# Kernel optimization log

Measured on AMD Instinct MI355X. Metric: run time of the kernel, lower is better.

The kernel has to match this reference:

```python
import jax, jax.numpy as jnp
import numpy as np

N_NODES = 50000
N_EDGES = 800000
IN_C, HID_C, OUT_C = 128, 96, 64
BN_EPS = 1e-5


def setup_inputs() -> dict:
    key = jax.random.key(0)
    ks = jax.random.split(key, 12)
    x = jax.random.normal(ks[0], (N_NODES, IN_C), dtype=jnp.float32)
    edge_weight = jax.random.uniform(ks[1], (N_EDGES,), dtype=jnp.float32)
    row = jax.random.randint(ks[2], (N_EDGES,), 0, N_NODES, dtype=jnp.int32)
    col = jax.random.randint(ks[3], (N_EDGES,), 0, N_NODES, dtype=jnp.int32)
    s = 0.05
    W1 = jax.random.normal(ks[4], (IN_C, HID_C), dtype=jnp.float32) * s
    b1 = jnp.zeros((HID_C,), dtype=jnp.float32)
    W2 = jax.random.normal(ks[5], (HID_C, HID_C), dtype=jnp.float32) * s
    b2 = jnp.zeros((HID_C,), dtype=jnp.float32)
    W3 = jax.random.normal(ks[6], (HID_C, OUT_C), dtype=jnp.float32) * s
    b3 = jnp.zeros((OUT_C,), dtype=jnp.float32)
    g1 = jnp.ones((HID_C,), dtype=jnp.float32)
    be1 = jnp.zeros((HID_C,), dtype=jnp.float32)
    g2 = jnp.ones((HID_C,), dtype=jnp.float32)
    be2 = jnp.zeros((HID_C,), dtype=jnp.float32)
    return {"x": x, "edge_weight": edge_weight, "row": row, "col": col,
            "W1": W1, "b1": b1, "W2": W2, "b2": b2, "W3": W3, "b3": b3,
            "g1": g1, "be1": be1, "g2": g2, "be2": be2}


def _gcn_conv(h, edge_weight, row, col, W, b):
    # GCNConv: adj_norm @ (h @ W) + b, adj in COO with normalized edge_weight
    h = h @ W  # [N, d_out]
    msg = edge_weight[:, None] * h[col]  # gather + scale: [E, d_out]
    agg = jax.ops.segment_sum(msg, row, num_segments=N_NODES)  # scatter-add
    return agg + b


def _batch_norm(h, gamma, beta):
    # BatchNorm1d (training-mode batch statistics, biased variance)
    mean = jnp.mean(h, axis=0)
    var = jnp.var(h, axis=0)
    return (h - mean) * jax.lax.rsqrt(var + BN_EPS) * gamma + beta


def reference(x, edge_weight, row, col, W1, b1, W2, b2, W3, b3, g1, be1, g2, be2):
    h = _gcn_conv(x, edge_weight, row, col, W1, b1)
    h = jax.nn.relu(_batch_norm(h, g1, be1))  # dropout is identity in eval
    h = _gcn_conv(h, edge_weight, row, col, W2, b2)
    h = jax.nn.relu(_batch_norm(h, g2, be2))
    h = _gcn_conv(h, edge_weight, row, col, W3, b3)
    return jax.nn.log_softmax(h, axis=-1)
```

## Files before the change

kernel.cpp:

```cpp
#include <hip/hip_runtime.h>
#include <hip/hip_bf16.h>
#include <math.h>

#define N_NODES 50000
#define N_EDGES 800000
#define IN_C 128
#define HID_C 96
#define OUT_C 64
#define BN_EPS 1e-5f

#define ELL_SHIFT 6
#define ELL_CAP   64

#define NGRP 8
#define GRP_ROWS ((N_NODES + NGRP - 1) / NGRP)

#define EW_SCALE 65535.0f
#define EW_INV   (1.0f / 65535.0f)

#define ST_SLICES 4

typedef __attribute__((ext_vector_type(8))) short short8;
typedef __attribute__((ext_vector_type(4))) float f32x4;

static __device__ __forceinline__ unsigned short f2b(float f) {
    __hip_bfloat16 b = __float2bfloat16(f);
    return *reinterpret_cast<unsigned short*>(&b);
}
static __device__ __forceinline__ float b2f(unsigned short u) {
    return __uint_as_float((unsigned)u << 16);
}
static __device__ __forceinline__ unsigned pack2(float a, float b) {
    return (unsigned)f2b(a) | ((unsigned)f2b(b) << 16);
}

#define FMA8(B, V, W)                                          \
    acc[(B) + 0] += (W) * __uint_as_float((V).x << 16);        \
    acc[(B) + 1] += (W) * __uint_as_float((V).x & 0xffff0000u);\
    acc[(B) + 2] += (W) * __uint_as_float((V).y << 16);        \
    acc[(B) + 3] += (W) * __uint_as_float((V).y & 0xffff0000u);\
    acc[(B) + 4] += (W) * __uint_as_float((V).z << 16);        \
    acc[(B) + 5] += (W) * __uint_as_float((V).z & 0xffff0000u);\
    acc[(B) + 6] += (W) * __uint_as_float((V).w << 16);        \
    acc[(B) + 7] += (W) * __uint_as_float((V).w & 0xffff0000u);

__global__ void prep_all(const float* __restrict__ W1, const float* __restrict__ W2,
                         const float* __restrict__ W3,
                         unsigned short* __restrict__ Wt1,
                         unsigned short* __restrict__ Wt2,
                         unsigned short* __restrict__ Wt3,
                         int* __restrict__ cnt, float* __restrict__ stats) {
    int i = blockIdx.x * blockDim.x + threadIdx.x;
    const int n1 = IN_C * HID_C, n2 = HID_C * HID_C, n3 = HID_C * OUT_C;
    if (i < n1) {
        int j = i / IN_C, k = i % IN_C;
        Wt1[i] = f2b(W1[k * HID_C + j]);
    } else if (i < n1 + n2) {
        int t = i - n1, j = t / HID_C, k = t % HID_C;
        Wt2[t] = f2b(W2[k * HID_C + j]);
    } else if (i < n1 + n2 + n3) {
        int t = i - n1 - n2, j = t / HID_C, k = t % HID_C;
        Wt3[t] = f2b(W3[k * OUT_C + j]);
    }
    if (i < N_NODES) cnt[i] = 0;
    if (i < 2 * ST_SLICES * 2 * HID_C) stats[i] = 0.f;
}

__global__ __launch_bounds__(256)
void fill_ell(const int* __restrict__ row, const int* __restrict__ col,
              const float* __restrict__ ew, int* __restrict__ cnt,
              unsigned int* __restrict__ pairs) {
    int g = blockIdx.x & (NGRP - 1);
    int e = (blockIdx.x >> 3) * 256 + threadIdx.x;
    if (e >= N_EDGES) return;
    int r = row[e];
    int lo = g * GRP_ROWS;
    if ((unsigned)(r - lo) >= (unsigned)GRP_ROWS) return;
    int slot = atomicAdd(&cnt[r], 1);
    if (slot < ELL_CAP) {
        unsigned wq = (unsigned)(ew[e] * EW_SCALE + 0.5f);
        pairs[((size_t)r << ELL_SHIFT) + slot] =
            (wq << 16) | (unsigned)col[e];
    }
}

template <int K, int J, bool APPLY, bool XBF16>
__global__ __launch_bounds__(256)
void gemm_mfma(const void* __restrict__ xin,
               const unsigned short* __restrict__ Wt,
               const float* __restrict__ stats,
               const float* __restrict__ gamma,
               const float* __restrict__ beta,
               unsigned short* __restrict__ h, int N) {
    constexpr int MT = 64;
    constexpr int SK = K + 8;
    constexpr int NT = J / 16;
    __shared__ unsigned short Xs[MT * SK];
    __shared__ unsigned short Ws[J * SK];
    __shared__ float scsh_s[APPLY ? 2 * K : 2];

    int tid = threadIdx.x;
    int tileBase = blockIdx.x * MT;

    if (APPLY) {
        if (tid < K) {
            float s = 0.f, sq = 0.f;
#pragma unroll
            for (int sl = 0; sl < ST_SLICES; ++sl) {
                s  += stats[sl * 2 * K + tid];
                sq += stats[sl * 2 * K + K + tid];
            }
            const float invN = 1.f / N_NODES;
            float mean = s * invN;
            float var = sq * invN - mean * mean;
            float sc = gamma[tid] * rsqrtf(var + BN_EPS);
            scsh_s[tid] = sc;
            scsh_s[K + tid] = beta[tid] - mean * sc;
        }
        __syncthreads();
    }

    if (XBF16) {
        const unsigned short* xb = (const unsigned short*)xin;
        for (int i = tid; i < MT * (K / 8); i += 256) {
            int node = i / (K / 8), kq = i % (K / 8);
            int gn = min(tileBase + node, N - 1);
            const unsigned short* src = xb + (size_t)gn * K + kq * 8;
            ushort4 u0 = *(const ushort4*)(src);
            ushort4 u1 = *(const ushort4*)(src + 4);
            if (APPLY) {
                int kb = kq * 8;
                float v0 = fmaxf(b2f(u0.x) * scsh_s[kb + 0] + scsh_s[K + kb + 0], 0.f);
                float v1 = fmaxf(b2f(u0.y) * scsh_s[kb + 1] + scsh_s[K + kb + 1], 0.f);
                float v2 = fmaxf(b2f(u0.z) * scsh_s[kb + 2] + scsh_s[K + kb + 2], 0.f);
                float v3 = fmaxf(b2f(u0.w) * scsh_s[kb + 3] + scsh_s[K + kb + 3], 0.f);
                float v4 = fmaxf(b2f(u1.x) * scsh_s[kb + 4] + scsh_s[K + kb + 4], 0.f);
                float v5 = fmaxf(b2f(u1.y) * scsh_s[kb + 5] + scsh_s[K + kb + 5], 0.f);
                float v6 = fmaxf(b2f(u1.z) * scsh_s[kb + 6] + scsh_s[K + kb + 6], 0.f);
                float v7 = fmaxf(b2f(u1.w) * scsh_s[kb + 7] + scsh_s[K + kb + 7], 0.f);
                u0 = make_ushort4(f2b(v0), f2b(v1), f2b(v2), f2b(v3));
                u1 = make_ushort4(f2b(v4), f2b(v5), f2b(v6), f2b(v7));
            }
            *(ushort4*)&Xs[node * SK + kq * 8] = u0;
            *(ushort4*)&Xs[node * SK + kq * 8 + 4] = u1;
        }
    } else {
        const float* xf = (const float*)xin;
        for (int i = tid; i < MT * (K / 4); i += 256) {
            int node = i / (K / 4), kq = i % (K / 4);
            int gn = min(tileBase + node, N - 1);
            float4 v = *(const float4*)(xf + (size_t)gn * K + kq * 4);
            ushort4 o = make_ushort4(f2b(v.x), f2b(v.y), f2b(v.z), f2b(v.w));
            *(ushort4*)&Xs[node * SK + kq * 4] = o;
        }
    }
    for (int i = tid; i < J * (K / 4); i += 256) {
        int j = i / (K / 4), kq = i % (K / 4);
        *(ushort4*)&Ws[j * SK + kq * 4] =
            *(const ushort4*)(Wt + (size_t)j * K + kq * 4);
    }
    __syncthreads();

    int lane = tid & 63;
    int w = tid >> 6;
    int m16 = lane & 15;
    int quad = lane >> 4;

    f32x4 acc[NT];
#pragma unroll
    for (int nt = 0; nt < NT; ++nt) acc[nt] = (f32x4){0.f, 0.f, 0.f, 0.f};

    const unsigned short* xrow = &Xs[(w * 16 + m16) * SK];
#pragma unroll
    for (int k0 = 0; k0 < K; k0 += 32) {
        short8 a = *(const short8*)(xrow + k0 + quad * 8);
#pragma unroll
        for (int nt = 0; nt < NT; ++nt) {
            short8 b = *(const short8*)&Ws[(nt * 16 + m16) * SK + k0 + quad * 8];
            acc[nt] = __builtin_amdgcn_mfma_f32_16x16x32_bf16(a, b, acc[nt], 0, 0, 0);
        }
    }

#pragma unroll
    for (int nt = 0; nt < NT; ++nt) {
#pragma unroll
        for (int r = 0; r < 4; ++r) {
            int node = tileBase + w * 16 + quad * 4 + r;
            if (node < N)
                h[(size_t)node * J + nt * 16 + m16] = f2b(acc[nt][r]);
        }
    }
}

template <int D, bool LSM, bool STATS>
__global__ __launch_bounds__(256)
void agg_fused(const unsigned short* __restrict__ h,
               const int* __restrict__ cnt,
               const unsigned int* __restrict__ pairs,
               unsigned short* __restrict__ outb,
               float* __restrict__ outf,
               const float* __restrict__ b3,
               float* __restrict__ stats) {
    constexpr int TPN = 4;
    constexpr int C = D / TPN;
    constexpr int NPB = 256 / TPN;
    __shared__ float shS[STATS ? 16 * C : 1];
    __shared__ float shQ[STATS ? 16 * C : 1];

    int tid = threadIdx.x;
    int q = tid & 3;
    int nloc = tid >> 2;
    int n = blockIdx.x * NPB + nloc;
    bool valid = n < N_NODES;
    int nn = valid ? n : N_NODES - 1;
    int end = valid ? min(cnt[nn], ELL_CAP) : 0;
    const unsigned* ep = pairs + ((size_t)nn << ELL_SHIFT);
    const int cbase = q * C;

    float acc[C];
#pragma unroll
    for (int c = 0; c < C; ++c) acc[c] = 0.f;

    int i = 0;
    for (; i + 1 < end; i += 2) {
        unsigned p0 = ep[i], p1 = ep[i + 1];
        float w0 = (float)(p0 >> 16) * EW_INV;
        float w1 = (float)(p1 >> 16) * EW_INV;
        const unsigned short* r0 = h + (size_t)(p0 & 0xFFFFu) * D + cbase;
        const unsigned short* r1 = h + (size_t)(p1 & 0xFFFFu) * D + cbase;
        uint4 v0[C / 8], v1[C / 8];
#pragma unroll
        for (int ch = 0; ch < C / 8; ++ch) v0[ch] = *(const uint4*)(r0 + ch * 8);
#pragma unroll
        for (int ch = 0; ch < C / 8; ++ch) v1[ch] = *(const uint4*)(r1 + ch * 8);
#pragma unroll
        for (int ch = 0; ch < C / 8; ++ch) { FMA8(ch * 8, v0[ch], w0) }
#pragma unroll
        for (int ch = 0; ch < C / 8; ++ch) { FMA8(ch * 8, v1[ch], w1) }
    }
    if (i < end) {
        unsigned p0 = ep[i];
        float w0 = (float)(p0 >> 16) * EW_INV;
        const unsigned short* r0 = h + (size_t)(p0 & 0xFFFFu) * D + cbase;
#pragma unroll
        for (int ch = 0; ch < C / 8; ++ch) {
            uint4 v = *(const uint4*)(r0 + ch * 8);
            FMA8(ch * 8, v, w0)
        }
    }

    if (LSM) {
        float v[C];
#pragma unroll
        for (int c = 0; c < C; ++c) v[c] = acc[c] + b3[cbase + c];
        float m = v[0];
#pragma unroll
        for (int c = 1; c < C; ++c) m = fmaxf(m, v[c]);
        m = fmaxf(m, __shfl_xor(m, 1));
        m = fmaxf(m, __shfl_xor(m, 2));
        float s = 0.f;
#pragma unroll
        for (int c = 0; c < C; ++c) s += expf(v[c] - m);
        s += __shfl_xor(s, 1);
        s += __shfl_xor(s, 2);
        float l = m + logf(s);
        if (valid) {
#pragma unroll
            for (int ch = 0; ch < C / 4; ++ch) {
                float4 o = make_float4(v[ch * 4 + 0] - l, v[ch * 4 + 1] - l,
                                       v[ch * 4 + 2] - l, v[ch * 4 + 3] - l);
                *(float4*)(outf + (size_t)n * D + cbase + ch * 4) = o;
            }
        }
    } else {
#pragma unroll
        for (int c = 0; c < C; ++c) acc[c] = b2f(f2b(acc[c]));
#pragma unroll
        for (int ch = 0; ch < C / 8; ++ch) {
            uint4 o;
            o.x = pack2(acc[ch * 8 + 0], acc[ch * 8 + 1]);
            o.y = pack2(acc[ch * 8 + 2], acc[ch * 8 + 3]);
            o.z = pack2(acc[ch * 8 + 4], acc[ch * 8 + 5]);
            o.w = pack2(acc[ch * 8 + 6], acc[ch * 8 + 7]);
            if (valid)
                *(uint4*)(outb + (size_t)n * D + cbase + ch * 8) = o;
        }
        if (STATS) {
            int lane = tid & 63;
            int wv = tid >> 6;
#pragma unroll
            for (int c = 0; c < C; ++c) {
                float s = acc[c];
                float sq = s * s;
#pragma unroll
                for (int msk = 4; msk < 64; msk <<= 1) {
                    s  += __shfl_xor(s, msk);
                    sq += __shfl_xor(sq, msk);
                }
                if (lane < 4) {
                    shS[(wv * 4 + lane) * C + c] = s;
                    shQ[(wv * 4 + lane) * C + c] = sq;
                }
            }
            __syncthreads();
            if (tid < D) {
                int qq = tid / C, cl = tid % C;
                float S = 0.f, Q = 0.f;
#pragma unroll
                for (int w2 = 0; w2 < 4; ++w2) {
                    S += shS[(w2 * 4 + qq) * C + cl];
                    Q += shQ[(w2 * 4 + qq) * C + cl];
                }
                int slice = blockIdx.x & (ST_SLICES - 1);
                atomicAdd(&stats[slice * 2 * D + tid], S);
                atomicAdd(&stats[slice * 2 * D + D + tid], Q);
            }
        }
    }
}

extern "C" void kernel_launch(void* const* d_in, const int* in_sizes, int n_in,
                              void* d_out, int out_size, void* d_ws, size_t ws_size,
                              hipStream_t stream) {
    const float* x   = (const float*)d_in[0];
    const float* ew  = (const float*)d_in[1];
    const int*   row = (const int*)d_in[2];
    const int*   col = (const int*)d_in[3];
    const float* W1  = (const float*)d_in[4];
    const float* W2  = (const float*)d_in[6];
    const float* W3  = (const float*)d_in[8];
    const float* b3  = (const float*)d_in[9];
    const float* g1  = (const float*)d_in[10];
    const float* be1 = (const float*)d_in[11];
    const float* g2  = (const float*)d_in[12];
    const float* be2 = (const float*)d_in[13];
    float* out = (float*)d_out;

    unsigned short* B      = (unsigned short*)d_ws;
    unsigned short* A      = B + (size_t)N_NODES * HID_C;
    unsigned short* Wt1    = A + (size_t)N_NODES * HID_C;
    unsigned short* Wt2    = Wt1 + IN_C * HID_C;
    unsigned short* Wt3    = Wt2 + HID_C * HID_C;
    unsigned int*   pairs  = (unsigned int*)(Wt3 + HID_C * OUT_C);
    int*            cnt    = (int*)(pairs + ((size_t)N_NODES << ELL_SHIFT));
    float*          stats1 = (float*)(cnt + N_NODES);
    float*          stats2 = stats1 + ST_SLICES * 2 * HID_C;

    const int T = 256;
    const int gridE  = (N_EDGES + T - 1) / T;
    const int gridG  = (N_NODES + 63) / 64;
    const int gridP  = (N_NODES + T - 1) / T;

    prep_all<<<gridP, T, 0, stream>>>(W1, W2, W3, Wt1, Wt2, Wt3, cnt, stats1);
    fill_ell<<<gridE * NGRP, T, 0, stream>>>(row, col, ew, cnt, pairs);

    gemm_mfma<IN_C, HID_C, false, false><<<gridG, T, 0, stream>>>(
        x, Wt1, nullptr, nullptr, nullptr, A, N_NODES);
    agg_fused<HID_C, false, true><<<gridG, T, 0, stream>>>(
        A, cnt, pairs, B, nullptr, nullptr, stats1);

    gemm_mfma<HID_C, HID_C, true, true><<<gridG, T, 0, stream>>>(
        B, Wt2, stats1, g1, be1, A, N_NODES);
    agg_fused<HID_C, false, true><<<gridG, T, 0, stream>>>(
        A, cnt, pairs, B, nullptr, nullptr, stats2);

    gemm_mfma<HID_C, OUT_C, true, true><<<gridG, T, 0, stream>>>(
        B, Wt3, stats2, g2, be2, A, N_NODES);
    agg_fused<OUT_C, true, false><<<gridG, T, 0, stream>>>(
        A, cnt, pairs, nullptr, out, b3, nullptr);
}
```

Before: 266.2 us.

## Split aggregation into specialized kernels with eight threads per node and 4-edge unroll

```diff
diff --git a/kernel.cpp b/kernel.cpp
--- a/kernel.cpp
+++ b/kernel.cpp
@@ -43,6 +43,12 @@
     acc[(B) + 5] += (W) * __uint_as_float((V).z & 0xffff0000u);\
     acc[(B) + 6] += (W) * __uint_as_float((V).w << 16);        \
     acc[(B) + 7] += (W) * __uint_as_float((V).w & 0xffff0000u);
+
+#define FMA4(B, V, W)                                          \
+    acc[(B) + 0] += (W) * __uint_as_float((V).x << 16);        \
+    acc[(B) + 1] += (W) * __uint_as_float((V).x & 0xffff0000u);\
+    acc[(B) + 2] += (W) * __uint_as_float((V).y << 16);        \
+    acc[(B) + 3] += (W) * __uint_as_float((V).y & 0xffff0000u);
 
 __global__ void prep_all(const float* __restrict__ W1, const float* __restrict__ W2,
                          const float* __restrict__ W3,
@@ -79,8 +85,7 @@
     int slot = atomicAdd(&cnt[r], 1);
     if (slot < ELL_CAP) {
         unsigned wq = (unsigned)(ew[e] * EW_SCALE + 0.5f);
-        pairs[((size_t)r << ELL_SHIFT) + slot] =
-            (wq << 16) | (unsigned)col[e];
+        pairs[((size_t)r << ELL_SHIFT) + slot] = (wq << 16) | (unsigned)col[e];
     }
 }
 
@@ -192,25 +197,17 @@
     }
 }
 
-template <int D, bool LSM, bool STATS>
 __global__ __launch_bounds__(256)
-void agg_fused(const unsigned short* __restrict__ h,
-               const int* __restrict__ cnt,
-               const unsigned int* __restrict__ pairs,
-               unsigned short* __restrict__ outb,
-               float* __restrict__ outf,
-               const float* __restrict__ b3,
-               float* __restrict__ stats) {
-    constexpr int TPN = 4;
-    constexpr int C = D / TPN;
-    constexpr int NPB = 256 / TPN;
-    __shared__ float shS[STATS ? 16 * C : 1];
-    __shared__ float shQ[STATS ? 16 * C : 1];
-
+void agg96(const unsigned short* __restrict__ h,
+           const int* __restrict__ cnt,
+           const unsigned int* __restrict__ pairs,
+           unsigned short* __restrict__ outb,
+           float* __restrict__ stats) {
+    constexpr int D = HID_C, C = 12;
     int tid = threadIdx.x;
-    int q = tid & 3;
-    int nloc = tid >> 2;
-    int n = blockIdx.x * NPB + nloc;
+    int q = tid & 7;
+    int nloc = tid >> 3;
+    int n = blockIdx.x * 32 + nloc;
     bool valid = n < N_NODES;
     int nn = valid ? n : N_NODES - 1;
     int end = valid ? min(cnt[nn], ELL_CAP) : 0;
@@ -222,100 +219,139 @@
     for (int c = 0; c < C; ++c) acc[c] = 0.f;
 
     int i = 0;
-    for (; i + 1 < end; i += 2) {
-        unsigned p0 = ep[i], p1 = ep[i + 1];
-        float w0 = (float)(p0 >> 16) * EW_INV;
-        float w1 = (float)(p1 >> 16) * EW_INV;
-        const unsigned short* r0 = h + (size_t)(p0 & 0xFFFFu) * D + cbase;
-        const unsigned short* r1 = h + (size_t)(p1 & 0xFFFFu) * D + cbase;
-        uint4 v0[C / 8], v1[C / 8];
-#pragma unroll
-        for (int ch = 0; ch < C / 8; ++ch) v0[ch] = *(const uint4*)(r0 + ch * 8);
-#pragma unroll
-        for (int ch = 0; ch < C / 8; ++ch) v1[ch] = *(const uint4*)(r1 + ch * 8);
-#pragma unroll
-        for (int ch = 0; ch < C / 8; ++ch) { FMA8(ch * 8, v0[ch], w0) }
-#pragma unroll
-        for (int ch = 0; ch < C / 8; ++ch) { FMA8(ch * 8, v1[ch], w1) }
-    }
-    if (i < end) {
-        unsigned p0 = ep[i];
-        float w0 = (float)(p0 >> 16) * EW_INV;
-        const unsigned short* r0 = h + (size_t)(p0 & 0xFFFFu) * D + cbase;
-#pragma unroll
-        for (int ch = 0; ch < C / 8; ++ch) {
-            uint4 v = *(const uint4*)(r0 + ch * 8);
-            FMA8(ch * 8, v, w0)
-        }
-    }
-
-    if (LSM) {
-        float v[C];
-#pragma unroll
-        for (int c = 0; c < C; ++c) v[c] = acc[c] + b3[cbase + c];
-        float m = v[0];
-#pragma unroll
-        for (int c = 1; c < C; ++c) m = fmaxf(m, v[c]);
-        m = fmaxf(m, __shfl_xor(m, 1));
-        m = fmaxf(m, __shfl_xor(m, 2));
-        float s = 0.f;
-#pragma unroll
-        for (int c = 0; c < C; ++c) s += expf(v[c] - m);
-        s += __shfl_xor(s, 1);
-        s += __shfl_xor(s, 2);
-        float l = m + logf(s);
-        if (valid) {
-#pragma unroll
-            for (int ch = 0; ch < C / 4; ++ch) {
-                float4 o = make_float4(v[ch * 4 + 0] - l, v[ch * 4 + 1] - l,
-                                       v[ch * 4 + 2] - l, v[ch * 4 + 3] - l);
-                *(float4*)(outf + (size_t)n * D + cbase + ch * 4) = o;
-            }
-        }
-    } else {
-#pragma unroll
-        for (int c = 0; c < C; ++c) acc[c] = b2f(f2b(acc[c]));
-#pragma unroll
-        for (int ch = 0; ch < C / 8; ++ch) {
-            uint4 o;
-            o.x = pack2(acc[ch * 8 + 0], acc[ch * 8 + 1]);
-            o.y = pack2(acc[ch * 8 + 2], acc[ch * 8 + 3]);
-            o.z = pack2(acc[ch * 8 + 4], acc[ch * 8 + 5]);
-            o.w = pack2(acc[ch * 8 + 6], acc[ch * 8 + 7]);
-            if (valid)
-                *(uint4*)(outb + (size_t)n * D + cbase + ch * 8) = o;
-        }
-        if (STATS) {
-            int lane = tid & 63;
-            int wv = tid >> 6;
-#pragma unroll
-            for (int c = 0; c < C; ++c) {
-                float s = acc[c];
-                float sq = s * s;
-#pragma unroll
-                for (int msk = 4; msk < 64; msk <<= 1) {
-                    s  += __shfl_xor(s, msk);
-                    sq += __shfl_xor(sq, msk);
-                }
-                if (lane < 4) {
-                    shS[(wv * 4 + lane) * C + c] = s;
-                    shQ[(wv * 4 + lane) * C + c] = sq;
-                }
-            }
-            __syncthreads();
-            if (tid < D) {
-                int qq = tid / C, cl = tid % C;
-                float S = 0.f, Q = 0.f;
-#pragma unroll
-                for (int w2 = 0; w2 < 4; ++w2) {
-                    S += shS[(w2 * 4 + qq) * C + cl];
-                    Q += shQ[(w2 * 4 + qq) * C + cl];
-                }
-                int slice = blockIdx.x & (ST_SLICES - 1);
-                atomicAdd(&stats[slice * 2 * D + tid], S);
-                atomicAdd(&stats[slice * 2 * D + D + tid], Q);
-            }
-        }
+    for (; i + 3 < end; i += 4) {
+        uint4 p = *(const uint4*)(ep + i);
+        float w0 = (float)(p.x >> 16) * EW_INV;
+        float w1 = (float)(p.y >> 16) * EW_INV;
+        float w2 = (float)(p.z >> 16) * EW_INV;
+        float w3 = (float)(p.w >> 16) * EW_INV;
+        const unsigned short* r0 = h + (size_t)(p.x & 0xFFFFu) * D + cbase;
+        const unsigned short* r1 = h + (size_t)(p.y & 0xFFFFu) * D + cbase;
+        const unsigned short* r2 = h + (size_t)(p.z & 0xFFFFu) * D + cbase;
+        const unsigned short* r3 = h + (size_t)(p.w & 0xFFFFu) * D + cbase;
+        uint2 a0 = *(const uint2*)(r0), a1 = *(const uint2*)(r0 + 4), a2 = *(const uint2*)(r0 + 8);
+        uint2 b0 = *(const uint2*)(r1), b1 = *(const uint2*)(r1 + 4), b2 = *(const uint2*)(r1 + 8);
+        uint2 c0 = *(const uint2*)(r2), c1 = *(const uint2*)(r2 + 4), c2 = *(const uint2*)(r2 + 8);
+        uint2 d0 = *(const uint2*)(r3), d1 = *(const uint2*)(r3 + 4), d2 = *(const uint2*)(r3 + 8);
+        FMA4(0, a0, w0) FMA4(4, a1, w0) FMA4(8, a2, w0)
+        FMA4(0, b0, w1) FMA4(4, b1, w1) FMA4(8, b2, w1)
+        FMA4(0, c0, w2) FMA4(4, c1, w2) FMA4(8, c2, w2)
+        FMA4(0, d0, w3) FMA4(4, d1, w3) FMA4(8, d2, w3)
+    }
+    for (; i < end; ++i) {
+        unsigned p = ep[i];
+        float w = (float)(p >> 16) * EW_INV;
+        const unsigned short* r0 = h + (size_t)(p & 0xFFFFu) * D + cbase;
+        uint2 a0 = *(const uint2*)(r0), a1 = *(const uint2*)(r0 + 4), a2 = *(const uint2*)(r0 + 8);
+        FMA4(0, a0, w) FMA4(4, a1, w) FMA4(8, a2, w)
+    }
+
+#pragma unroll
+    for (int c = 0; c < C; ++c) acc[c] = b2f(f2b(acc[c]));
+
+    if (valid) {
+        unsigned short* dst = outb + (size_t)n * D + cbase;
+        uint2 o0, o1, o2;
+        o0.x = pack2(acc[0], acc[1]);   o0.y = pack2(acc[2], acc[3]);
+        o1.x = pack2(acc[4], acc[5]);   o1.y = pack2(acc[6], acc[7]);
+        o2.x = pack2(acc[8], acc[9]);   o2.y = pack2(acc[10], acc[11]);
+        *(uint2*)(dst) = o0; *(uint2*)(dst + 4) = o1; *(uint2*)(dst + 8) = o2;
+    }
+
+    __shared__ float shS[4 * 8 * C];
+    __shared__ float shQ[4 * 8 * C];
+    int lane = tid & 63, wv = tid >> 6;
+#pragma unroll
+    for (int c = 0; c < C; ++c) {
+        float s = acc[c];
+        float sq = s * s;
+        s  += __shfl_xor(s, 8);  sq += __shfl_xor(sq, 8);
+        s  += __shfl_xor(s, 16); sq += __shfl_xor(sq, 16);
+        s  += __shfl_xor(s, 32); sq += __shfl_xor(sq, 32);
+        if (lane < 8) { shS[(wv * 8 + lane) * C + c] = s;
+                        shQ[(wv * 8 + lane) * C + c] = sq; }
+    }
+    __syncthreads();
+    if (tid < D) {
+        int qq = tid / C, cl = tid % C;
+        float S = 0.f, Q = 0.f;
+#pragma unroll
+        for (int w2 = 0; w2 < 4; ++w2) {
+            S += shS[(w2 * 8 + qq) * C + cl];
+            Q += shQ[(w2 * 8 + qq) * C + cl];
+        }
+        int sl = blockIdx.x & (ST_SLICES - 1);
+        atomicAdd(&stats[sl * 2 * D + tid], S);
+        atomicAdd(&stats[sl * 2 * D + D + tid], Q);
+    }
+}
+
+__global__ __launch_bounds__(256)
+void agg64_lsm(const unsigned short* __restrict__ h,
+               const int* __restrict__ cnt,
+               const unsigned int* __restrict__ pairs,
+               float* __restrict__ outf,
+               const float* __restrict__ b3) {
+    constexpr int D = OUT_C, C = 8;
+    int tid = threadIdx.x;
+    int q = tid & 7;
+    int nloc = tid >> 3;
+    int n = blockIdx.x * 32 + nloc;
+    bool valid = n < N_NODES;
+    int nn = valid ? n : N_NODES - 1;
+    int end = valid ? min(cnt[nn], ELL_CAP) : 0;
+    const unsigned* ep = pairs + ((size_t)nn << ELL_SHIFT);
+    const int cbase = q * C;
+
+    float acc[C];
+#pragma unroll
+    for (int c = 0; c < C; ++c) acc[c] = 0.f;
+
+    int i = 0;
+    for (; i + 3 < end; i += 4) {
+        uint4 p = *(const uint4*)(ep + i);
+        float w0 = (float)(p.x >> 16) * EW_INV;
+        float w1 = (float)(p.y >> 16) * EW_INV;
+        float w2 = (float)(p.z >> 16) * EW_INV;
+        float w3 = (float)(p.w >> 16) * EW_INV;
+        uint4 v0 = *(const uint4*)(h + (size_t)(p.x & 0xFFFFu) * D + cbase);
+        uint4 v1 = *(const uint4*)(h + (size_t)(p.y & 0xFFFFu) * D + cbase);
+        uint4 v2 = *(const uint4*)(h + (size_t)(p.z & 0xFFFFu) * D + cbase);
+        uint4 v3 = *(const uint4*)(h + (size_t)(p.w & 0xFFFFu) * D + cbase);
+        FMA8(0, v0, w0)
+        FMA8(0, v1, w1)
+        FMA8(0, v2, w2)
+        FMA8(0, v3, w3)
+    }
+    for (; i < end; ++i) {
+        unsigned p = ep[i];
+        float w = (float)(p >> 16) * EW_INV;
+        uint4 v = *(const uint4*)(h + (size_t)(p & 0xFFFFu) * D + cbase);
+        FMA8(0, v, w)
+    }
+
+    float v[C];
+#pragma unroll
+    for (int c = 0; c < C; ++c) v[c] = acc[c] + b3[cbase + c];
+    float m = v[0];
+#pragma unroll
+    for (int c = 1; c < C; ++c) m = fmaxf(m, v[c]);
+    m = fmaxf(m, __shfl_xor(m, 1));
+    m = fmaxf(m, __shfl_xor(m, 2));
+    m = fmaxf(m, __shfl_xor(m, 4));
+    float s = 0.f;
+#pragma unroll
+    for (int c = 0; c < C; ++c) s += expf(v[c] - m);
+    s += __shfl_xor(s, 1);
+    s += __shfl_xor(s, 2);
+    s += __shfl_xor(s, 4);
+    float l = m + logf(s);
+    if (valid) {
+        float4 o0 = make_float4(v[0] - l, v[1] - l, v[2] - l, v[3] - l);
+        float4 o1 = make_float4(v[4] - l, v[5] - l, v[6] - l, v[7] - l);
+        float* dst = outf + (size_t)n * D + cbase;
+        *(float4*)(dst) = o0;
+        *(float4*)(dst + 4) = o1;
     }
 }
 
@@ -349,6 +385,7 @@
     const int T = 256;
     const int gridE  = (N_EDGES + T - 1) / T;
     const int gridG  = (N_NODES + 63) / 64;
+    const int gridA  = (N_NODES + 31) / 32;
     const int gridP  = (N_NODES + T - 1) / T;
 
     prep_all<<<gridP, T, 0, stream>>>(W1, W2, W3, Wt1, Wt2, Wt3, cnt, stats1);
@@ -356,16 +393,13 @@
 
     gemm_mfma<IN_C, HID_C, false, false><<<gridG, T, 0, stream>>>(
         x, Wt1, nullptr, nullptr, nullptr, A, N_NODES);
-    agg_fused<HID_C, false, true><<<gridG, T, 0, stream>>>(
-        A, cnt, pairs, B, nullptr, nullptr, stats1);
+    agg96<<<gridA, T, 0, stream>>>(A, cnt, pairs, B, stats1);
 
     gemm_mfma<HID_C, HID_C, true, true><<<gridG, T, 0, stream>>>(
         B, Wt2, stats1, g1, be1, A, N_NODES);
-    agg_fused<HID_C, false, true><<<gridG, T, 0, stream>>>(
-        A, cnt, pairs, B, nullptr, nullptr, stats2);
+    agg96<<<gridA, T, 0, stream>>>(A, cnt, pairs, B, stats2);
 
     gemm_mfma<HID_C, OUT_C, true, true><<<gridG, T, 0, stream>>>(
         B, Wt3, stats2, g2, be2, A, N_NODES);
-    agg_fused<OUT_C, true, false><<<gridG, T, 0, stream>>>(
-        A, cnt, pairs, nullptr, out, b3, nullptr);
-}
+    agg64_lsm<<<gridA, T, 0, stream>>>(A, cnt, pairs, out, b3);
+}
```

Measured after the change: 256.6 us. 3.6% less time.
